# Kernel optimization log

Measured on AMD Instinct MI355X. Metric: run time of the kernel, lower is better.

The kernel has to match this reference:

```python
import jax, jax.numpy as jnp
import numpy as np


def conv1x1(x, w, b):
    # x: [B,Ci,H,W], w: [Co,Ci,1,1], b: [Co]
    return jnp.einsum('bihw,oi->bohw', x, w[:, :, 0, 0]) + b[None, :, None, None]


def guide_nn(x, w1, b1, w2, b2):
    h = jax.nn.relu(conv1x1(x, w1, b1))
    return jnp.tanh(conv1x1(h, w2, b2))


def trilinear_slice(grid, gx, gy, gz):
    # grid: [B,C,D,Gh,Gw]; gx,gy,gz: [B,H,W] in ~[-1,1]
    B, C, D, Gh, Gw = grid.shape
    fx = jnp.clip((gx + 1.0) * 0.5 * (Gw - 1), 0.0, Gw - 1)
    fy = jnp.clip((gy + 1.0) * 0.5 * (Gh - 1), 0.0, Gh - 1)
    fz = jnp.clip((gz + 1.0) * 0.5 * (D - 1), 0.0, D - 1)
    x0 = jnp.floor(fx).astype(jnp.int32); x1 = jnp.minimum(x0 + 1, Gw - 1)
    y0 = jnp.floor(fy).astype(jnp.int32); y1 = jnp.minimum(y0 + 1, Gh - 1)
    z0 = jnp.floor(fz).astype(jnp.int32); z1 = jnp.minimum(z0 + 1, D - 1)
    wx = (fx - x0)[:, None]; wy = (fy - y0)[:, None]; wz = (fz - z0)[:, None]

    gather = jax.vmap(lambda g, zi, yi, xi: g[:, zi, yi, xi])  # -> [B,C,H,W]

    out = (
        gather(grid, z0, y0, x0) * (1 - wz) * (1 - wy) * (1 - wx)
        + gather(grid, z0, y0, x1) * (1 - wz) * (1 - wy) * wx
        + gather(grid, z0, y1, x0) * (1 - wz) * wy * (1 - wx)
        + gather(grid, z0, y1, x1) * (1 - wz) * wy * wx
        + gather(grid, z1, y0, x0) * wz * (1 - wy) * (1 - wx)
        + gather(grid, z1, y0, x1) * wz * (1 - wy) * wx
        + gather(grid, z1, y1, x0) * wz * wy * (1 - wx)
        + gather(grid, z1, y1, x1) * wz * wy * wx
    )
    return out


def slicing(grid, guide):
    # guide: [B,1,H,W] (single-channel context map)
    B, c, H, W = guide.shape
    x = (jnp.arange(W, dtype=guide.dtype) - W / 2) / (W / 2)
    y = (jnp.arange(H, dtype=guide.dtype) - H / 2) / (H / 2)
    yy, xx = jnp.meshgrid(y, x, indexing='ij')
    gx = jnp.broadcast_to(xx[None], (B, H, W))
    gy = jnp.broadcast_to(yy[None], (B, H, W))
    gz = guide[:, 0]
    return trilinear_slice(grid, gx, gy, gz)


def apply_coefficent(x, coeff):
    # x: [B,Ci,H,W]; coeff: [B,Co,Ci+1,H,W] -> per-pixel affine
    ci = x.shape[1]
    return jnp.einsum('boihw,bihw->bohw', coeff[:, :, :ci], x) + coeff[:, :, ci]


def setup_inputs() -> dict:
    key = jax.random.key(0)
    ks = jax.random.split(key, 12)
    B, H, W = 8, 512, 512
    D, Gh, Gw = 8, 16, 16
    inp = {
        'src': jax.random.uniform(ks[0], (B, 3, H, W), jnp.float32),
        'grid1': jax.random.normal(ks[1], (B, 32, D, Gh, Gw), jnp.float32),
        'grid2': jax.random.normal(ks[2], (B, 27, D, Gh, Gw), jnp.float32),
        'w1': jax.random.normal(ks[3], (16, 3, 1, 1), jnp.float32) * 0.1,
        'b1': jnp.zeros((16,), jnp.float32),
        'w2': jax.random.normal(ks[4], (1, 16, 1, 1), jnp.float32) * 0.1,
        'b2': jnp.zeros((1,), jnp.float32),
        'w3': jax.random.normal(ks[5], (16, 8, 1, 1), jnp.float32) * 0.1,
        'b3': jnp.zeros((16,), jnp.float32),
        'w4': jax.random.normal(ks[6], (1, 16, 1, 1), jnp.float32) * 0.1,
        'b4': jnp.zeros((1,), jnp.float32),
    }
    return inp


def reference(src, grid1, grid2, w1, b1, w2, b2, w3, b3, w4, b4):
    B, _, H, W = src.shape
    context_map = guide_nn(src, w1, b1, w2, b2)            # [B,1,H,W]
    coeff1 = slicing(grid1, context_map)                    # [B,32,H,W]
    coeff1_split = jnp.transpose(coeff1.reshape(B, 4, 8, H, W), (0, 2, 1, 3, 4))  # [B,8,4,H,W]
    hidden = jax.nn.relu(apply_coefficent(src, coeff1_split))  # [B,8,H,W]
    context_map2 = guide_nn(hidden, w3, b3, w4, b4)         # [B,1,H,W]
    coeff2 = slicing(grid2, context_map2)                   # [B,27,H,W]
    coeff2_split = jnp.transpose(coeff2.reshape(B, 9, 3, H, W), (0, 2, 1, 3, 4))  # [B,3,9,H,W]
    out = apply_coefficent(hidden, coeff2_split)            # [B,3,H,W]
    return out
```

## Files before the change

kernel.cpp:

```cpp
#include <hip/hip_runtime.h>
#include <math.h>

#define BATCH 8
#define IMH 512
#define IMW 512
#define HWSZ (IMH * IMW)
#define XSPAN 9
#define CH 32
#define CPADH 40
#define L_CELLS (XSPAN * 8)
#define LSLOTH (L_CELLS * CPADH)

typedef _Float16 h1;
typedef _Float16 h2 __attribute__((ext_vector_type(2)));

union V16 {
    uint4 u;
    h2 h[4];
};

__device__ __forceinline__ float fast_tanh(float x) {
    float e = __expf(2.0f * x);
    return fmaf(-2.0f, __builtin_amdgcn_rcpf(e + 1.0f), 1.0f);
}

__global__ __launch_bounds__(256) void transpose_both(const float* __restrict__ g1,
                                                      const float* __restrict__ g2,
                                                      h1* __restrict__ t1,
                                                      h1* __restrict__ t2) {
    int idx = blockIdx.x * 256 + threadIdx.x;
    if (idx < 524288) {
        int x = idx & 15, y = (idx >> 4) & 15, z = (idx >> 8) & 7;
        int c = (idx >> 11) & 31, b = idx >> 16;
        t1[((((b * 16 + y) * 16 + x) * 8 + z) << 5) + c] = (h1)g1[idx];
    } else if (idx < 966656) {
        int j = idx - 524288;
        int x = j & 15, y = (j >> 4) & 15, z = (j >> 8) & 7;
        int r = j >> 11;
        int c = r % 27, b = r / 27;
        t2[((((b * 16 + y) * 16 + x) * 8 + z) << 5) + c] = (h1)g2[j];
    } else {
        int k = idx - 966656;
        int cell = k / 5, p = k - cell * 5;
        t2[(cell << 5) + 27 + p] = (h1)0.0f;
    }
}

template <bool TR>
__global__ __launch_bounds__(256, 4) void fused4(
    const float* __restrict__ src,
    const void* __restrict__ g1p,
    const void* __restrict__ g2p,
    const float* __restrict__ w1, const float* __restrict__ b1,
    const float* __restrict__ w2, const float* __restrict__ b2,
    const float* __restrict__ w3, const float* __restrict__ b3,
    const float* __restrict__ w4, const float* __restrict__ b4,
    float* __restrict__ out) {
    __shared__ __align__(16) h1 L1h[LSLOTH];
    __shared__ __align__(16) h1 L2h[LSLOTH];

    int tid = threadIdx.x;
    int half_ = blockIdx.x & 1;
    int h = (blockIdx.x >> 1) & 511;
    int b = blockIdx.x >> 10;
    int w0 = half_ << 8;
    int x_lo = half_ ? 7 : 0;

    float fy = (float)h * (15.0f / 512.0f);
    int y0 = (int)fy;
    float wy = fy - (float)y0;

    if (TR) {
        h2 wyh = (h2)(h1)wy;
        {
            const uint4* pa = (const uint4*)((const h1*)g1p +
                              ((((size_t)b * 16 + y0) * 16 + x_lo) * 8) * CH);
            const uint4* pb = pa + (16 * 8 * CH) / 8;
            for (int t = tid; t < L_CELLS * 4; t += 256) {
                int g = t & 3, cell = t >> 2;
                V16 v0, v1, r;
                v0.u = pa[t];
                v1.u = pb[t];
#pragma unroll
                for (int k = 0; k < 4; ++k) r.h[k] = v0.h[k] + (v1.h[k] - v0.h[k]) * wyh;
                *(uint4*)&L1h[cell * CPADH + 8 * g] = r.u;
            }
        }
        {
            const uint4* pa = (const uint4*)((const h1*)g2p +
                              ((((size_t)b * 16 + y0) * 16 + x_lo) * 8) * CH);
            const uint4* pb = pa + (16 * 8 * CH) / 8;
            for (int t = tid; t < L_CELLS * 4; t += 256) {
                int g = t & 3, cell = t >> 2;
                V16 v0, v1, r;
                v0.u = pa[t];
                v1.u = pb[t];
#pragma unroll
                for (int k = 0; k < 4; ++k) r.h[k] = v0.h[k] + (v1.h[k] - v0.h[k]) * wyh;
                *(uint4*)&L2h[cell * CPADH + 8 * g] = r.u;
            }
        }
    } else {
        const float* g1f = (const float*)g1p;
        const float* g2f = (const float*)g2p;
        for (int t = tid; t < L_CELLS * CH; t += 256) {
            int c = t & 31, cell = t >> 5;
            int z = cell & 7, xj = cell >> 3;
            size_t o0 = ((((size_t)b * 32 + c) * 8 + z) * 16 + y0) * 16 + (x_lo + xj);
            float v0 = g1f[o0], v1 = g1f[o0 + 16];
            L1h[cell * CPADH + c] = (h1)fmaf(wy, v1 - v0, v0);
        }
        for (int t = tid; t < L_CELLS * CH; t += 256) {
            int c = t & 31, cell = t >> 5;
            int z = cell & 7, xj = cell >> 3;
            float v = 0.0f;
            if (c < 27) {
                size_t o0 = ((((size_t)b * 27 + c) * 8 + z) * 16 + y0) * 16 + (x_lo + xj);
                v = fmaf(wy, g2f[o0 + 16] - g2f[o0], g2f[o0]);
            }
            L2h[cell * CPADH + c] = (h1)v;
        }
    }
    __syncthreads();

    int w = w0 + tid;
    const float* sb = src + (size_t)b * 3 * HWSZ + h * IMW + w;
    float s0 = sb[0];
    float s1 = sb[HWSZ];
    float s2 = sb[2 * HWSZ];

    float acc = b2[0];
#pragma unroll
    for (int j = 0; j < 16; ++j) {
        float t = fmaf(w1[j * 3 + 0], s0,
                  fmaf(w1[j * 3 + 1], s1,
                  fmaf(w1[j * 3 + 2], s2, b1[j])));
        acc = fmaf(w2[j], fmaxf(t, 0.0f), acc);
    }
    float fz = fmaf(fast_tanh(acc), 3.5f, 3.5f);
    fz = fminf(fmaxf(fz, 0.0f), 7.0f);
    int z0 = min((int)fz, 6);
    float wz = fz - (float)z0;

    float fx = (float)w * (15.0f / 512.0f);
    int x0 = (int)fx;
    float wx = fx - (float)x0;
    int a00 = ((x0 - x_lo) * 8 + z0) * CPADH;

    float w11v = wx * wz;
    float w10v = wx - w11v;
    float w01v = wz - w11v;
    float w00v = 1.0f - wx - wz + w11v;
    h2 W00 = (h2)(h1)w00v, W01 = (h2)(h1)w01v, W10 = (h2)(h1)w10v, W11 = (h2)(h1)w11v;

    const uint4* p00 = (const uint4*)&L1h[a00];
    const uint4* p01 = (const uint4*)&L1h[a00 + CPADH];
    const uint4* p10 = (const uint4*)&L1h[a00 + 8 * CPADH];
    const uint4* p11 = (const uint4*)&L1h[a00 + 9 * CPADH];
    float c1f[32];
#pragma unroll
    for (int j = 0; j < 4; ++j) {
        V16 A, B, C, D;
        A.u = p00[j];
        B.u = p01[j];
        C.u = p10[j];
        D.u = p11[j];
#pragma unroll
        for (int k = 0; k < 4; ++k) {
            h2 r = A.h[k] * W00 + B.h[k] * W01 + C.h[k] * W10 + D.h[k] * W11;
            c1f[j * 8 + 2 * k]     = (float)r[0];
            c1f[j * 8 + 2 * k + 1] = (float)r[1];
        }
    }

    float hid[8];
#pragma unroll
    for (int o = 0; o < 8; ++o) {
        float t = fmaf(c1f[o], s0,
                  fmaf(c1f[8 + o], s1,
                  fmaf(c1f[16 + o], s2, c1f[24 + o])));
        hid[o] = fmaxf(t, 0.0f);
    }

    float acc2 = b4[0];
#pragma unroll
    for (int j = 0; j < 16; ++j) {
        float t = b3[j];
#pragma unroll
        for (int i = 0; i < 8; ++i) t = fmaf(w3[j * 8 + i], hid[i], t);
        acc2 = fmaf(w4[j], fmaxf(t, 0.0f), acc2);
    }
    float fz2 = fmaf(fast_tanh(acc2), 3.5f, 3.5f);
    fz2 = fminf(fmaxf(fz2, 0.0f), 7.0f);
    int z0b = min((int)fz2, 6);
    float wz2 = fz2 - (float)z0b;

    int a00b = ((x0 - x_lo) * 8 + z0b) * CPADH;
    float u11 = wx * wz2;
    float u10 = wx - u11;
    float u01 = wz2 - u11;
    float u00 = 1.0f - wx - wz2 + u11;
    h2 U00 = (h2)(h1)u00, U01 = (h2)(h1)u01, U10 = (h2)(h1)u10, U11 = (h2)(h1)u11;

    const uint4* q00 = (const uint4*)&L2h[a00b];
    const uint4* q01 = (const uint4*)&L2h[a00b + CPADH];
    const uint4* q10 = (const uint4*)&L2h[a00b + 8 * CPADH];
    const uint4* q11 = (const uint4*)&L2h[a00b + 9 * CPADH];
    float c2f[27];
#pragma unroll
    for (int j = 0; j < 4; ++j) {
        V16 A, B, C, D;
        A.u = q00[j];
        B.u = q01[j];
        C.u = q10[j];
        D.u = q11[j];
#pragma unroll
        for (int k = 0; k < 4; ++k) {
            h2 r = A.h[k] * U00 + B.h[k] * U01 + C.h[k] * U10 + D.h[k] * U11;
            int c = j * 8 + 2 * k;
            if (c < 27)     c2f[c]     = (float)r[0];
            if (c + 1 < 27) c2f[c + 1] = (float)r[1];
        }
    }

    float* ob = out + (size_t)b * 3 * HWSZ + h * IMW + w;
#pragma unroll
    for (int o = 0; o < 3; ++o) {
        float t = c2f[24 + o];
#pragma unroll
        for (int i = 0; i < 8; ++i) t = fmaf(c2f[i * 3 + o], hid[i], t);
        ob[(size_t)o * HWSZ] = t;
    }
}

extern "C" void kernel_launch(void* const* d_in, const int* in_sizes, int n_in,
                              void* d_out, int out_size, void* d_ws, size_t ws_size,
                              hipStream_t stream) {
    const float* src   = (const float*)d_in[0];
    const float* grid1 = (const float*)d_in[1];
    const float* grid2 = (const float*)d_in[2];
    const float* w1 = (const float*)d_in[3];
    const float* b1 = (const float*)d_in[4];
    const float* w2 = (const float*)d_in[5];
    const float* b2 = (const float*)d_in[6];
    const float* w3 = (const float*)d_in[7];
    const float* b3 = (const float*)d_in[8];
    const float* w4 = (const float*)d_in[9];
    const float* b4 = (const float*)d_in[10];
    float* out = (float*)d_out;

    const size_t t_elems = (size_t)BATCH * 2048 * CH;
    const size_t ws_needed = 2 * t_elems * sizeof(h1);

    const int nblk = (BATCH * HWSZ) / 256;

    if (ws_size >= ws_needed) {
        h1* t1 = (h1*)d_ws;
        h1* t2 = t1 + t_elems;
        transpose_both<<<4096, 256, 0, stream>>>(grid1, grid2, t1, t2);
        fused4<true><<<nblk, 256, 0, stream>>>(
            src, t1, t2, w1, b1, w2, b2, w3, b3, w4, b4, out);
    } else {
        fused4<false><<<nblk, 256, 0, stream>>>(
            src, grid1, grid2, w1, b1, w2, b2, w3, b3, w4, b4, out);
    }
}
```

Before: 125.8 us.

## Process full image row per block, staging all grid columns in LDS

Each block now handles a whole 512-pixel row with two pixels per thread instead of half a row, so the y-interpolated grid slice is loaded into LDS once per row rather than twice. The LDS slab grows from 9 to 16 x-cells, and the src loads for both pixels are issued before the grid staging so they overlap with it. The trade-offs are half as many blocks, more LDS per block (which may reduce occupancy), and more registers per thread.

```diff
diff --git a/kernel.cpp b/kernel.cpp
--- a/kernel.cpp
+++ b/kernel.cpp
@@ -5,10 +5,9 @@
 #define IMH 512
 #define IMW 512
 #define HWSZ (IMH * IMW)
-#define XSPAN 9
 #define CH 32
 #define CPADH 40
-#define L_CELLS (XSPAN * 8)
+#define L_CELLS (16 * 8)
 #define LSLOTH (L_CELLS * CPADH)
 
 typedef _Float16 h1;
@@ -47,7 +46,7 @@
 }
 
 template <bool TR>
-__global__ __launch_bounds__(256, 4) void fused4(
+__global__ __launch_bounds__(256, 4) void fused5(
     const float* __restrict__ src,
     const void* __restrict__ g1p,
     const void* __restrict__ g2p,
@@ -60,45 +59,36 @@
     __shared__ __align__(16) h1 L2h[LSLOTH];
 
     int tid = threadIdx.x;
-    int half_ = blockIdx.x & 1;
-    int h = (blockIdx.x >> 1) & 511;
-    int b = blockIdx.x >> 10;
-    int w0 = half_ << 8;
-    int x_lo = half_ ? 7 : 0;
+    int h = blockIdx.x & 511;
+    int b = blockIdx.x >> 9;
 
     float fy = (float)h * (15.0f / 512.0f);
     int y0 = (int)fy;
     float wy = fy - (float)y0;
 
+    const float* sbase = src + (size_t)b * 3 * HWSZ + (size_t)h * IMW;
+    float sA0 = sbase[tid],           sA1 = sbase[HWSZ + tid],       sA2 = sbase[2 * HWSZ + tid];
+    float sB0 = sbase[tid + 256],     sB1 = sbase[HWSZ + tid + 256], sB2 = sbase[2 * HWSZ + tid + 256];
+
     if (TR) {
         h2 wyh = (h2)(h1)wy;
-        {
-            const uint4* pa = (const uint4*)((const h1*)g1p +
-                              ((((size_t)b * 16 + y0) * 16 + x_lo) * 8) * CH);
-            const uint4* pb = pa + (16 * 8 * CH) / 8;
-            for (int t = tid; t < L_CELLS * 4; t += 256) {
-                int g = t & 3, cell = t >> 2;
-                V16 v0, v1, r;
-                v0.u = pa[t];
-                v1.u = pb[t];
-#pragma unroll
-                for (int k = 0; k < 4; ++k) r.h[k] = v0.h[k] + (v1.h[k] - v0.h[k]) * wyh;
-                *(uint4*)&L1h[cell * CPADH + 8 * g] = r.u;
-            }
-        }
-        {
-            const uint4* pa = (const uint4*)((const h1*)g2p +
-                              ((((size_t)b * 16 + y0) * 16 + x_lo) * 8) * CH);
-            const uint4* pb = pa + (16 * 8 * CH) / 8;
-            for (int t = tid; t < L_CELLS * 4; t += 256) {
-                int g = t & 3, cell = t >> 2;
-                V16 v0, v1, r;
-                v0.u = pa[t];
-                v1.u = pb[t];
-#pragma unroll
-                for (int k = 0; k < 4; ++k) r.h[k] = v0.h[k] + (v1.h[k] - v0.h[k]) * wyh;
-                *(uint4*)&L2h[cell * CPADH + 8 * g] = r.u;
-            }
+        const uint4* p1 = (const uint4*)g1p + ((size_t)b * 16 + y0) * 512;
+        const uint4* p2 = (const uint4*)g2p + ((size_t)b * 16 + y0) * 512;
+#pragma unroll
+        for (int t = tid; t < 512; t += 256) {
+            int g = t & 3, cell = t >> 2;
+            V16 v0, v1, r0;
+            v0.u = p1[t];
+            v1.u = p1[t + 512];
+#pragma unroll
+            for (int k = 0; k < 4; ++k) r0.h[k] = v0.h[k] + (v1.h[k] - v0.h[k]) * wyh;
+            *(uint4*)&L1h[cell * CPADH + 8 * g] = r0.u;
+            V16 u0, u1, r1;
+            u0.u = p2[t];
+            u1.u = p2[t + 512];
+#pragma unroll
+            for (int k = 0; k < 4; ++k) r1.h[k] = u0.h[k] + (u1.h[k] - u0.h[k]) * wyh;
+            *(uint4*)&L2h[cell * CPADH + 8 * g] = r1.u;
         }
     } else {
         const float* g1f = (const float*)g1p;
@@ -106,7 +96,7 @@
         for (int t = tid; t < L_CELLS * CH; t += 256) {
             int c = t & 31, cell = t >> 5;
             int z = cell & 7, xj = cell >> 3;
-            size_t o0 = ((((size_t)b * 32 + c) * 8 + z) * 16 + y0) * 16 + (x_lo + xj);
+            size_t o0 = ((((size_t)b * 32 + c) * 8 + z) * 16 + y0) * 16 + xj;
             float v0 = g1f[o0], v1 = g1f[o0 + 16];
             L1h[cell * CPADH + c] = (h1)fmaf(wy, v1 - v0, v0);
         }
@@ -115,7 +105,7 @@
             int z = cell & 7, xj = cell >> 3;
             float v = 0.0f;
             if (c < 27) {
-                size_t o0 = ((((size_t)b * 27 + c) * 8 + z) * 16 + y0) * 16 + (x_lo + xj);
+                size_t o0 = ((((size_t)b * 27 + c) * 8 + z) * 16 + y0) * 16 + xj;
                 v = fmaf(wy, g2f[o0 + 16] - g2f[o0], g2f[o0]);
             }
             L2h[cell * CPADH + c] = (h1)v;
@@ -123,113 +113,115 @@
     }
     __syncthreads();
 
-    int w = w0 + tid;
-    const float* sb = src + (size_t)b * 3 * HWSZ + h * IMW + w;
-    float s0 = sb[0];
-    float s1 = sb[HWSZ];
-    float s2 = sb[2 * HWSZ];
-
-    float acc = b2[0];
-#pragma unroll
-    for (int j = 0; j < 16; ++j) {
-        float t = fmaf(w1[j * 3 + 0], s0,
-                  fmaf(w1[j * 3 + 1], s1,
-                  fmaf(w1[j * 3 + 2], s2, b1[j])));
-        acc = fmaf(w2[j], fmaxf(t, 0.0f), acc);
-    }
-    float fz = fmaf(fast_tanh(acc), 3.5f, 3.5f);
-    fz = fminf(fmaxf(fz, 0.0f), 7.0f);
-    int z0 = min((int)fz, 6);
-    float wz = fz - (float)z0;
-
-    float fx = (float)w * (15.0f / 512.0f);
-    int x0 = (int)fx;
-    float wx = fx - (float)x0;
-    int a00 = ((x0 - x_lo) * 8 + z0) * CPADH;
-
-    float w11v = wx * wz;
-    float w10v = wx - w11v;
-    float w01v = wz - w11v;
-    float w00v = 1.0f - wx - wz + w11v;
-    h2 W00 = (h2)(h1)w00v, W01 = (h2)(h1)w01v, W10 = (h2)(h1)w10v, W11 = (h2)(h1)w11v;
-
-    const uint4* p00 = (const uint4*)&L1h[a00];
-    const uint4* p01 = (const uint4*)&L1h[a00 + CPADH];
-    const uint4* p10 = (const uint4*)&L1h[a00 + 8 * CPADH];
-    const uint4* p11 = (const uint4*)&L1h[a00 + 9 * CPADH];
-    float c1f[32];
-#pragma unroll
-    for (int j = 0; j < 4; ++j) {
-        V16 A, B, C, D;
-        A.u = p00[j];
-        B.u = p01[j];
-        C.u = p10[j];
-        D.u = p11[j];
-#pragma unroll
-        for (int k = 0; k < 4; ++k) {
-            h2 r = A.h[k] * W00 + B.h[k] * W01 + C.h[k] * W10 + D.h[k] * W11;
-            c1f[j * 8 + 2 * k]     = (float)r[0];
-            c1f[j * 8 + 2 * k + 1] = (float)r[1];
-        }
-    }
-
-    float hid[8];
-#pragma unroll
-    for (int o = 0; o < 8; ++o) {
-        float t = fmaf(c1f[o], s0,
-                  fmaf(c1f[8 + o], s1,
-                  fmaf(c1f[16 + o], s2, c1f[24 + o])));
-        hid[o] = fmaxf(t, 0.0f);
-    }
-
-    float acc2 = b4[0];
-#pragma unroll
-    for (int j = 0; j < 16; ++j) {
-        float t = b3[j];
-#pragma unroll
-        for (int i = 0; i < 8; ++i) t = fmaf(w3[j * 8 + i], hid[i], t);
-        acc2 = fmaf(w4[j], fmaxf(t, 0.0f), acc2);
-    }
-    float fz2 = fmaf(fast_tanh(acc2), 3.5f, 3.5f);
-    fz2 = fminf(fmaxf(fz2, 0.0f), 7.0f);
-    int z0b = min((int)fz2, 6);
-    float wz2 = fz2 - (float)z0b;
-
-    int a00b = ((x0 - x_lo) * 8 + z0b) * CPADH;
-    float u11 = wx * wz2;
-    float u10 = wx - u11;
-    float u01 = wz2 - u11;
-    float u00 = 1.0f - wx - wz2 + u11;
-    h2 U00 = (h2)(h1)u00, U01 = (h2)(h1)u01, U10 = (h2)(h1)u10, U11 = (h2)(h1)u11;
-
-    const uint4* q00 = (const uint4*)&L2h[a00b];
-    const uint4* q01 = (const uint4*)&L2h[a00b + CPADH];
-    const uint4* q10 = (const uint4*)&L2h[a00b + 8 * CPADH];
-    const uint4* q11 = (const uint4*)&L2h[a00b + 9 * CPADH];
-    float c2f[27];
-#pragma unroll
-    for (int j = 0; j < 4; ++j) {
-        V16 A, B, C, D;
-        A.u = q00[j];
-        B.u = q01[j];
-        C.u = q10[j];
-        D.u = q11[j];
-#pragma unroll
-        for (int k = 0; k < 4; ++k) {
-            h2 r = A.h[k] * U00 + B.h[k] * U01 + C.h[k] * U10 + D.h[k] * U11;
-            int c = j * 8 + 2 * k;
-            if (c < 27)     c2f[c]     = (float)r[0];
-            if (c + 1 < 27) c2f[c + 1] = (float)r[1];
-        }
-    }
-
-    float* ob = out + (size_t)b * 3 * HWSZ + h * IMW + w;
-#pragma unroll
-    for (int o = 0; o < 3; ++o) {
-        float t = c2f[24 + o];
-#pragma unroll
-        for (int i = 0; i < 8; ++i) t = fmaf(c2f[i * 3 + o], hid[i], t);
-        ob[(size_t)o * HWSZ] = t;
+    float* obase = out + (size_t)b * 3 * HWSZ + (size_t)h * IMW;
+#pragma unroll 2
+    for (int p = 0; p < 2; ++p) {
+        int w = tid + (p << 8);
+        float s0 = p ? sB0 : sA0;
+        float s1 = p ? sB1 : sA1;
+        float s2 = p ? sB2 : sA2;
+
+        float acc = b2[0];
+#pragma unroll
+        for (int j = 0; j < 16; ++j) {
+            float t = fmaf(w1[j * 3 + 0], s0,
+                      fmaf(w1[j * 3 + 1], s1,
+                      fmaf(w1[j * 3 + 2], s2, b1[j])));
+            acc = fmaf(w2[j], fmaxf(t, 0.0f), acc);
+        }
+        float fz = fmaf(fast_tanh(acc), 3.5f, 3.5f);
+        fz = fminf(fmaxf(fz, 0.0f), 7.0f);
+        int z0 = min((int)fz, 6);
+        float wz = fz - (float)z0;
+
+        float fx = (float)w * (15.0f / 512.0f);
+        int x0 = (int)fx;
+        float wx = fx - (float)x0;
+        int a00 = (x0 * 8 + z0) * CPADH;
+
+        float w11v = wx * wz;
+        float w10v = wx - w11v;
+        float w01v = wz - w11v;
+        float w00v = 1.0f - wx - wz + w11v;
+        h2 W00 = (h2)(h1)w00v, W01 = (h2)(h1)w01v, W10 = (h2)(h1)w10v, W11 = (h2)(h1)w11v;
+
+        const uint4* p00 = (const uint4*)&L1h[a00];
+        const uint4* p01 = (const uint4*)&L1h[a00 + CPADH];
+        const uint4* p10 = (const uint4*)&L1h[a00 + 8 * CPADH];
+        const uint4* p11 = (const uint4*)&L1h[a00 + 9 * CPADH];
+        float c1f[32];
+#pragma unroll
+        for (int j = 0; j < 4; ++j) {
+            V16 A, B, C, D;
+            A.u = p00[j];
+            B.u = p01[j];
+            C.u = p10[j];
+            D.u = p11[j];
+#pragma unroll
+            for (int k = 0; k < 4; ++k) {
+                h2 r = A.h[k] * W00 + B.h[k] * W01 + C.h[k] * W10 + D.h[k] * W11;
+                c1f[j * 8 + 2 * k]     = (float)r[0];
+                c1f[j * 8 + 2 * k + 1] = (float)r[1];
+            }
+        }
+
+        float hid[8];
+#pragma unroll
+        for (int o = 0; o < 8; ++o) {
+            float t = fmaf(c1f[o], s0,
+                      fmaf(c1f[8 + o], s1,
+                      fmaf(c1f[16 + o], s2, c1f[24 + o])));
+            hid[o] = fmaxf(t, 0.0f);
+        }
+
+        float acc2 = b4[0];
+#pragma unroll
+        for (int j = 0; j < 16; ++j) {
+            float t = b3[j];
+#pragma unroll
+            for (int i = 0; i < 8; ++i) t = fmaf(w3[j * 8 + i], hid[i], t);
+            acc2 = fmaf(w4[j], fmaxf(t, 0.0f), acc2);
+        }
+        float fz2 = fmaf(fast_tanh(acc2), 3.5f, 3.5f);
+        fz2 = fminf(fmaxf(fz2, 0.0f), 7.0f);
+        int z0b = min((int)fz2, 6);
+        float wz2 = fz2 - (float)z0b;
+
+        int a00b = (x0 * 8 + z0b) * CPADH;
+        float u11 = wx * wz2;
+        float u10 = wx - u11;
+        float u01 = wz2 - u11;
+        float u00 = 1.0f - wx - wz2 + u11;
+        h2 U00 = (h2)(h1)u00, U01 = (h2)(h1)u01, U10 = (h2)(h1)u10, U11 = (h2)(h1)u11;
+
+        const uint4* q00 = (const uint4*)&L2h[a00b];
+        const uint4* q01 = (const uint4*)&L2h[a00b + CPADH];
+        const uint4* q10 = (const uint4*)&L2h[a00b + 8 * CPADH];
+        const uint4* q11 = (const uint4*)&L2h[a00b + 9 * CPADH];
+        float c2f[27];
+#pragma unroll
+        for (int j = 0; j < 4; ++j) {
+            V16 A, B, C, D;
+            A.u = q00[j];
+            B.u = q01[j];
+            C.u = q10[j];
+            D.u = q11[j];
+#pragma unroll
+            for (int k = 0; k < 4; ++k) {
+                h2 r = A.h[k] * U00 + B.h[k] * U01 + C.h[k] * U10 + D.h[k] * U11;
+                int c = j * 8 + 2 * k;
+                if (c < 27)     c2f[c]     = (float)r[0];
+                if (c + 1 < 27) c2f[c + 1] = (float)r[1];
+            }
+        }
+
+#pragma unroll
+        for (int o = 0; o < 3; ++o) {
+            float t = c2f[24 + o];
+#pragma unroll
+            for (int i = 0; i < 8; ++i) t = fmaf(c2f[i * 3 + o], hid[i], t);
+            obase[(size_t)o * HWSZ + w] = t;
+        }
     }
 }
 
@@ -252,16 +244,16 @@
     const size_t t_elems = (size_t)BATCH * 2048 * CH;
     const size_t ws_needed = 2 * t_elems * sizeof(h1);
 
-    const int nblk = (BATCH * HWSZ) / 256;
+    const int nblk = BATCH * IMH;
 
     if (ws_size >= ws_needed) {
         h1* t1 = (h1*)d_ws;
         h1* t2 = t1 + t_elems;
         transpose_both<<<4096, 256, 0, stream>>>(grid1, grid2, t1, t2);
-        fused4<true><<<nblk, 256, 0, stream>>>(
+        fused5<true><<<nblk, 256, 0, stream>>>(
             src, t1, t2, w1, b1, w2, b2, w3, b3, w4, b4, out);
     } else {
-        fused4<false><<<nblk, 256, 0, stream>>>(
+        fused5<false><<<nblk, 256, 0, stream>>>(
             src, grid1, grid2, w1, b1, w2, b2, w3, b3, w4, b4, out);
     }
 }
```

Result: no change. 126.2 us (+0.3%).
